# Performance work log

Hardware: AMD Instinct MI355X
Metric: run time of the kernel (lower is better)

The kernel has to match this reference:

```python
import jax, jax.numpy as jnp
import numpy as np

D_MODEL = 512
NHEAD = 8
HEAD_DIM = D_MODEL // NHEAD
D_FF = 2048
EPS = 1e-5


def _layernorm(x, w, b):
    mu = jnp.mean(x, axis=-1, keepdims=True)
    var = jnp.mean(jnp.square(x - mu), axis=-1, keepdims=True)
    return (x - mu) * jax.lax.rsqrt(var + EPS) * w + b


def setup_inputs() -> dict:
    key = jax.random.key(0)
    ks = jax.random.split(key, 10)
    B, L = 4, 2048
    x = jax.random.normal(ks[0], (B, L, D_MODEL), dtype=jnp.float32)
    attn_bias = jax.random.normal(ks[1], (1, NHEAD, L, L), dtype=jnp.float32)
    s = 0.02
    # weights stored as (in, out): y = x @ w + b
    wq = jax.random.normal(ks[2], (D_MODEL, D_MODEL), dtype=jnp.float32) * s
    wk = jax.random.normal(ks[3], (D_MODEL, D_MODEL), dtype=jnp.float32) * s
    wv = jax.random.normal(ks[4], (D_MODEL, D_MODEL), dtype=jnp.float32) * s
    wo = jax.random.normal(ks[5], (D_MODEL, D_MODEL), dtype=jnp.float32) * s
    w1 = jax.random.normal(ks[6], (D_MODEL, D_FF), dtype=jnp.float32) * s
    w2 = jax.random.normal(ks[7], (D_FF, D_MODEL), dtype=jnp.float32) * s
    z = lambda n: jnp.zeros((n,), dtype=jnp.float32)
    o = lambda n: jnp.ones((n,), dtype=jnp.float32)
    return {
        "x": x, "attn_bias": attn_bias,
        "ln1_w": o(D_MODEL), "ln1_b": z(D_MODEL),
        "ln2_w": o(D_MODEL), "ln2_b": z(D_MODEL),
        "wq": wq, "bq": z(D_MODEL), "wk": wk, "bk": z(D_MODEL),
        "wv": wv, "bv": z(D_MODEL), "wo": wo, "bo": z(D_MODEL),
        "w1": w1, "b1": z(D_FF), "w2": w2, "b2": z(D_MODEL),
    }


def reference(x, attn_bias, ln1_w, ln1_b, ln2_w, ln2_b,
              wq, bq, wk, bk, wv, bv, wo, bo, w1, b1, w2, b2):
    B, L, D = x.shape
    H, Dh = NHEAD, HEAD_DIM

    # --- self-attention block (pre-LN) ---
    h = _layernorm(x, ln1_w, ln1_b)
    q = (h @ wq + bq).reshape(B, L, H, Dh)
    k = (h @ wk + bk).reshape(B, L, H, Dh)
    v = (h @ wv + bv).reshape(B, L, H, Dh)
    scores = jnp.einsum('bqhd,bkhd->bhqk', q, k) * (Dh ** -0.5)
    scores = scores + attn_bias  # broadcast over batch if bias has leading 1
    attn = jax.nn.softmax(scores, axis=-1)
    o = jnp.einsum('bhqk,bkhd->bqhd', attn, v).reshape(B, L, D)
    x = x + (o @ wo + bo)

    # --- feed-forward block (pre-LN, exact GELU like torch nn.GELU) ---
    h2 = _layernorm(x, ln2_w, ln2_b)
    ff = jax.nn.gelu(h2 @ w1 + b1, approximate=False) @ w2 + b2
    return x + ff
```

## Files before the change

### kernel.cpp

```cpp
#include <hip/hip_runtime.h>
#include <hip/hip_bf16.h>

typedef __bf16 bf16x8 __attribute__((ext_vector_type(8)));
typedef float  f32x4  __attribute__((ext_vector_type(4)));
typedef unsigned short us8 __attribute__((ext_vector_type(8)));

__device__ inline unsigned short f2bf(float f) {
    unsigned u = __builtin_bit_cast(unsigned, f);
    u += 0x7fffu + ((u >> 16) & 1u);
    return (unsigned short)(u >> 16);
}

__device__ inline bf16x8 load_frag(const unsigned short* p) {
    return *reinterpret_cast<const bf16x8*>(p);
}

__device__ inline void gload_lds16(const unsigned short* g, unsigned short* l) {
    __builtin_amdgcn_global_load_lds(
        (const __attribute__((address_space(1))) void*)g,
        (__attribute__((address_space(3))) void*)l, 16, 0, 0);
}

__global__ void prep_kernel(const float* __restrict__ wq, const float* __restrict__ wk,
                            const float* __restrict__ wv, const float* __restrict__ wo,
                            const float* __restrict__ w1, const float* __restrict__ w2,
                            const float* __restrict__ bq, const float* __restrict__ bk,
                            const float* __restrict__ bv,
                            unsigned short* __restrict__ wqkvT, unsigned short* __restrict__ woT,
                            unsigned short* __restrict__ w1T, unsigned short* __restrict__ w2T,
                            float* __restrict__ biasqkv) {
    int bid = blockIdx.x;
    int tx = threadIdx.x, ty = threadIdx.y;
    if (bid >= 3072) {
        int i = (bid - 3072) * 256 + ty * 32 + tx;
        float v = (i < 512) ? bq[i] : ((i < 1024) ? bk[i - 512] : bv[i - 1024]);
        biasqkv[i] = v;
        return;
    }
    const float* src; unsigned short* dst; int K, N, tile;
    if (bid < 256)       { src = wq; dst = wqkvT;          K = 512;  N = 512;  tile = bid; }
    else if (bid < 512)  { src = wk; dst = wqkvT + 262144; K = 512;  N = 512;  tile = bid - 256; }
    else if (bid < 768)  { src = wv; dst = wqkvT + 524288; K = 512;  N = 512;  tile = bid - 512; }
    else if (bid < 1024) { src = wo; dst = woT;            K = 512;  N = 512;  tile = bid - 768; }
    else if (bid < 2048) { src = w1; dst = w1T;            K = 512;  N = 2048; tile = bid - 1024; }
    else                 { src = w2; dst = w2T;            K = 2048; N = 512;  tile = bid - 2048; }
    int ntx = N >> 5;
    int n0 = (tile % ntx) * 32, k0 = (tile / ntx) * 32;
    __shared__ float tilebuf[32][33];
#pragma unroll
    for (int i = 0; i < 4; ++i)
        tilebuf[ty + 8 * i][tx] = src[(size_t)(k0 + ty + 8 * i) * N + n0 + tx];
    __syncthreads();
#pragma unroll
    for (int i = 0; i < 4; ++i)
        dst[(size_t)(n0 + ty + 8 * i) * K + k0 + tx] = f2bf(tilebuf[tx][ty + 8 * i]);
}

__global__ __launch_bounds__(256) void ln_kernel(const float* __restrict__ x,
                                                 const float* __restrict__ w,
                                                 const float* __restrict__ b,
                                                 unsigned short* __restrict__ out) {
    int wave = threadIdx.x >> 6, lane = threadIdx.x & 63;
    size_t row = (size_t)blockIdx.x * 4 + wave;
    const float* xp = x + row * 512 + lane * 8;
    float4 v0 = *reinterpret_cast<const float4*>(xp);
    float4 v1 = *reinterpret_cast<const float4*>(xp + 4);
    float s = (v0.x + v0.y) + (v0.z + v0.w) + (v1.x + v1.y) + (v1.z + v1.w);
    float qq = v0.x * v0.x + v0.y * v0.y + v0.z * v0.z + v0.w * v0.w
             + v1.x * v1.x + v1.y * v1.y + v1.z * v1.z + v1.w * v1.w;
#pragma unroll
    for (int off = 1; off < 64; off <<= 1) {
        s += __shfl_xor(s, off, 64);
        qq += __shfl_xor(qq, off, 64);
    }
    float mu = s * (1.0f / 512.0f);
    float var = qq * (1.0f / 512.0f) - mu * mu;
    float rstd = rsqrtf(var + 1e-5f);
    int c = lane * 8;
    float4 w0 = *reinterpret_cast<const float4*>(w + c);
    float4 w1 = *reinterpret_cast<const float4*>(w + c + 4);
    float4 b0 = *reinterpret_cast<const float4*>(b + c);
    float4 b1 = *reinterpret_cast<const float4*>(b + c + 4);
    us8 r;
    r[0] = f2bf((v0.x - mu) * rstd * w0.x + b0.x);
    r[1] = f2bf((v0.y - mu) * rstd * w0.y + b0.y);
    r[2] = f2bf((v0.z - mu) * rstd * w0.z + b0.z);
    r[3] = f2bf((v0.w - mu) * rstd * w0.w + b0.w);
    r[4] = f2bf((v1.x - mu) * rstd * w1.x + b1.x);
    r[5] = f2bf((v1.y - mu) * rstd * w1.y + b1.y);
    r[6] = f2bf((v1.z - mu) * rstd * w1.z + b1.z);
    r[7] = f2bf((v1.w - mu) * rstd * w1.w + b1.w);
    *reinterpret_cast<us8*>(out + row * 512 + c) = r;
}

__device__ __forceinline__ void gemm_core(const unsigned short* __restrict__ A,
                                          const unsigned short* __restrict__ BT,
                                          int K, int kbeg, int ksteps,
                                          int m0, int n0, f32x4 (&acc)[4][4]) {
    __shared__ unsigned short As[8192];
    __shared__ unsigned short Bs[8192];
    const int tid = threadIdx.x;
    const int lane = tid & 63, wave = tid >> 6;
    const int quad = lane >> 4, l16 = lane & 15;
    const int wm = (wave >> 1) * 64, wn = (wave & 1) * 64;
    const int row0 = tid >> 3;
    const int jl = (tid & 7) ^ (row0 & 7);
    const unsigned short* ag = A + (size_t)(m0 + row0) * K + kbeg + jl * 8;
    const unsigned short* bg = BT + (size_t)(n0 + row0) * K + kbeg + jl * 8;
    unsigned short* al = As + tid * 8;
    unsigned short* bl = Bs + tid * 8;
    const int sw = l16 & 7;

    for (int ks = 0; ks < ksteps; ++ks) {
        __syncthreads();
#pragma unroll
        for (int s = 0; s < 4; ++s) {
            gload_lds16(ag + (size_t)32 * s * K, al + 2048 * s);
            gload_lds16(bg + (size_t)32 * s * K, bl + 2048 * s);
        }
        ag += 64; bg += 64;
        __syncthreads();
#pragma unroll
        for (int h = 0; h < 2; ++h) {
            bf16x8 af[4], bf[4];
#pragma unroll
            for (int i = 0; i < 4; ++i)
                af[i] = load_frag(As + (wm + i * 16 + l16) * 64 + (((h * 4 + quad) ^ sw) * 8));
#pragma unroll
            for (int j = 0; j < 4; ++j)
                bf[j] = load_frag(Bs + (wn + j * 16 + l16) * 64 + (((h * 4 + quad) ^ sw) * 8));
#pragma unroll
            for (int i = 0; i < 4; ++i)
#pragma unroll
                for (int j = 0; j < 4; ++j)
                    acc[i][j] = __builtin_amdgcn_mfma_f32_16x16x32_bf16(af[i], bf[j], acc[i][j], 0, 0, 0);
        }
    }
}

__global__ __launch_bounds__(256, 3) void gemm_qkv_k(const unsigned short* __restrict__ A,
                                                     const unsigned short* __restrict__ BT,
                                                     const float* __restrict__ bias,
                                                     unsigned short* __restrict__ qk,
                                                     unsigned short* __restrict__ vT) {
    f32x4 acc[4][4] = {};
    const int m0 = blockIdx.y * 128, n0 = blockIdx.x * 128;
    gemm_core(A, BT, 512, 0, 8, m0, n0, acc);
    const int tid = threadIdx.x, lane = tid & 63, wave = tid >> 6;
    const int quad = lane >> 4, l16 = lane & 15;
    const int wm = (wave >> 1) * 64, wn = (wave & 1) * 64;
    if (n0 < 1024) {
#pragma unroll
        for (int i = 0; i < 4; ++i)
#pragma unroll
            for (int j = 0; j < 4; ++j) {
                int n = n0 + wn + j * 16 + l16;
                float bn = bias[n];
#pragma unroll
                for (int r = 0; r < 4; ++r) {
                    int m = m0 + wm + i * 16 + quad * 4 + r;
                    qk[(size_t)m * 1024 + n] = f2bf(acc[i][j][r] + bn);
                }
            }
    } else {
#pragma unroll
        for (int i = 0; i < 4; ++i) {
            int mb = m0 + wm + i * 16 + quad * 4;
            int bb = mb >> 11, tok = mb & 2047;
#pragma unroll
            for (int j = 0; j < 4; ++j) {
                int n = n0 + wn + j * 16 + l16;
                float bn = bias[n];
                int hd = n - 1024;
                ushort4 pk;
                pk.x = f2bf(acc[i][j][0] + bn);
                pk.y = f2bf(acc[i][j][1] + bn);
                pk.z = f2bf(acc[i][j][2] + bn);
                pk.w = f2bf(acc[i][j][3] + bn);
                *reinterpret_cast<ushort4*>(vT + (size_t)(bb * 512 + hd) * 2048 + tok) = pk;
            }
        }
    }
}

__global__ __launch_bounds__(256, 3) void gemm_gelu_k(const unsigned short* __restrict__ A,
                                                      const unsigned short* __restrict__ BT,
                                                      const float* __restrict__ bias,
                                                      unsigned short* __restrict__ C) {
    f32x4 acc[4][4] = {};
    const int m0 = blockIdx.y * 128, n0 = blockIdx.x * 128;
    gemm_core(A, BT, 512, 0, 8, m0, n0, acc);
    const int tid = threadIdx.x, lane = tid & 63, wave = tid >> 6;
    const int quad = lane >> 4, l16 = lane & 15;
    const int wm = (wave >> 1) * 64, wn = (wave & 1) * 64;
#pragma unroll
    for (int i = 0; i < 4; ++i)
#pragma unroll
        for (int j = 0; j < 4; ++j) {
            int n = n0 + wn + j * 16 + l16;
            float bn = bias[n];
#pragma unroll
            for (int r = 0; r < 4; ++r) {
                int m = m0 + wm + i * 16 + quad * 4 + r;
                float val = acc[i][j][r] + bn;
                float g = 0.5f * val * (1.0f + erff(val * 0.70710678118654752f));
                C[(size_t)m * 2048 + n] = f2bf(g);
            }
        }
}

__global__ __launch_bounds__(256, 3) void gemm_atomic_k(const unsigned short* __restrict__ A,
                                                        const unsigned short* __restrict__ BT,
                                                        const float* __restrict__ bias,
                                                        float* __restrict__ C,
                                                        int N, int K, int ksteps) {
    f32x4 acc[4][4] = {};
    const int m0 = blockIdx.y * 128, n0 = blockIdx.x * 128;
    const int kbeg = blockIdx.z * ksteps * 64;
    gemm_core(A, BT, K, kbeg, ksteps, m0, n0, acc);
    const int tid = threadIdx.x, lane = tid & 63, wave = tid >> 6;
    const int quad = lane >> 4, l16 = lane & 15;
    const int wm = (wave >> 1) * 64, wn = (wave & 1) * 64;
    const bool addb = (blockIdx.z == 0);
#pragma unroll
    for (int i = 0; i < 4; ++i)
#pragma unroll
        for (int j = 0; j < 4; ++j) {
            int n = n0 + wn + j * 16 + l16;
            float bn = addb ? bias[n] : 0.0f;
#pragma unroll
            for (int r = 0; r < 4; ++r) {
                int m = m0 + wm + i * 16 + quad * 4 + r;
                atomicAdd(&C[(size_t)m * N + n], acc[i][j][r] + bn);
            }
        }
}

__global__ __launch_bounds__(256, 4) void attn_kernel(const unsigned short* __restrict__ qk,
                                                      const unsigned short* __restrict__ vT,
                                                      const float* __restrict__ bias,
                                                      unsigned short* __restrict__ o) {
    __shared__ unsigned short Ks[2][4096];
    __shared__ unsigned short VTs[2][4096];
    __shared__ unsigned short Ps[4096];
    const int tid = threadIdx.x;
    const int lane = tid & 63, wave = tid >> 6, quad = lane >> 4, l16 = lane & 15;
    const int qb = blockIdx.x, h = blockIdx.y, b = blockIdx.z;
    const int qw = qb * 64 + wave * 16;

    const unsigned short* qbase = qk + (size_t)(b * 2048 + qw + l16) * 1024 + h * 64 + quad * 8;
    bf16x8 qf0 = load_frag(qbase);
    bf16x8 qf1 = load_frag(qbase + 32);

    f32x4 Oacc[4] = {};
    float lsum[4] = {};

    const int p8 = lane & 7;
    const int r0 = wave * 16 + (lane >> 3);
    const int swz = (p8 ^ (r0 & 7)) * 8;
    const unsigned short* kg = qk + (size_t)(b * 2048 + r0) * 1024 + 512 + h * 64 + swz;
    const unsigned short* vg = vT + (size_t)(b * 512 + h * 64 + r0) * 2048 + swz;
    const int ldst = r0 * 64 + p8 * 8;

    const float* brow = bias + (size_t)h * 2048 * 2048 + (size_t)(qw + quad * 4) * 2048 + l16;
    const float S2 = 0.18033688011112042f;
    const float K2 = 1.4426950408889634f;
    const float C2 = -11.541560327111707f;

    gload_lds16(kg, Ks[0] + ldst);
    gload_lds16(kg + 8 * 1024, Ks[0] + 512 + ldst);
    gload_lds16(vg, VTs[0] + ldst);
    gload_lds16(vg + 8 * 2048, VTs[0] + 512 + ldst);
    float bbf[4][4];
#pragma unroll
    for (int t = 0; t < 4; ++t)
#pragma unroll
        for (int r = 0; r < 4; ++r)
            bbf[t][r] = fmaf(brow[(size_t)r * 2048 + t * 16], K2, C2);

    const int sw7 = l16 & 7;
    for (int kt = 0; kt < 32; ++kt) {
        const int buf = kt & 1;
        __syncthreads();
        if (kt < 31) {
            const unsigned short* kg2 = kg + (size_t)(kt + 1) * 64 * 1024;
            const unsigned short* vg2 = vg + (kt + 1) * 64;
            gload_lds16(kg2, Ks[buf ^ 1] + ldst);
            gload_lds16(kg2 + 8 * 1024, Ks[buf ^ 1] + 512 + ldst);
            gload_lds16(vg2, VTs[buf ^ 1] + ldst);
            gload_lds16(vg2 + 8 * 2048, VTs[buf ^ 1] + 512 + ldst);
        }
#pragma unroll
        for (int t = 0; t < 4; ++t) {
            const unsigned short* krow = Ks[buf] + (t * 16 + l16) * 64;
            bf16x8 kb0 = load_frag(krow + ((quad ^ sw7) * 8));
            bf16x8 kb1 = load_frag(krow + (((quad + 4) ^ sw7) * 8));
            f32x4 c = {};
            c = __builtin_amdgcn_mfma_f32_16x16x32_bf16(qf0, kb0, c, 0, 0, 0);
            c = __builtin_amdgcn_mfma_f32_16x16x32_bf16(qf1, kb1, c, 0, 0, 0);
#pragma unroll
            for (int r = 0; r < 4; ++r) {
                float e = __builtin_amdgcn_exp2f(fmaf(c[r], S2, bbf[t][r]));
                lsum[r] += e;
                int m = quad * 4 + r;
                int phys = (t * 2 + (l16 >> 3)) ^ ((m >> 1) & 7);
                Ps[wave * 1024 + m * 64 + phys * 8 + (l16 & 7)] = f2bf(e);
            }
        }
        __syncthreads();
        if (kt < 31) {
            const float* b2 = brow + (size_t)(kt + 1) * 64;
#pragma unroll
            for (int t = 0; t < 4; ++t)
#pragma unroll
                for (int r = 0; r < 4; ++r)
                    bbf[t][r] = fmaf(b2[(size_t)r * 2048 + t * 16], K2, C2);
        }
        const unsigned short* prow = Ps + wave * 1024 + l16 * 64;
        bf16x8 pa0 = load_frag(prow + ((quad ^ ((l16 >> 1) & 7)) * 8));
        bf16x8 pa1 = load_frag(prow + (((quad + 4) ^ ((l16 >> 1) & 7)) * 8));
#pragma unroll
        for (int t = 0; t < 4; ++t) {
            const unsigned short* vrow = VTs[buf] + (t * 16 + l16) * 64;
            bf16x8 vb0 = load_frag(vrow + ((quad ^ sw7) * 8));
            bf16x8 vb1 = load_frag(vrow + (((quad + 4) ^ sw7) * 8));
            Oacc[t] = __builtin_amdgcn_mfma_f32_16x16x32_bf16(pa0, vb0, Oacc[t], 0, 0, 0);
            Oacc[t] = __builtin_amdgcn_mfma_f32_16x16x32_bf16(pa1, vb1, Oacc[t], 0, 0, 0);
        }
    }

#pragma unroll
    for (int off = 1; off < 16; off <<= 1)
#pragma unroll
        for (int r = 0; r < 4; ++r) lsum[r] += __shfl_xor(lsum[r], off, 64);
#pragma unroll
    for (int r = 0; r < 4; ++r) {
        float inv = 1.0f / lsum[r];
        int qg = qw + quad * 4 + r;
        unsigned short* op = o + (size_t)(b * 2048 + qg) * 512 + h * 64;
#pragma unroll
        for (int t = 0; t < 4; ++t) op[t * 16 + l16] = f2bf(Oacc[t][r] * inv);
    }
}

extern "C" void kernel_launch(void* const* d_in, const int* in_sizes, int n_in,
                              void* d_out, int out_size, void* d_ws, size_t ws_size,
                              hipStream_t stream) {
    const float* x      = (const float*)d_in[0];
    const float* abias  = (const float*)d_in[1];
    const float* ln1_w  = (const float*)d_in[2];
    const float* ln1_b  = (const float*)d_in[3];
    const float* ln2_w  = (const float*)d_in[4];
    const float* ln2_b  = (const float*)d_in[5];
    const float* wq     = (const float*)d_in[6];
    const float* bq     = (const float*)d_in[7];
    const float* wk     = (const float*)d_in[8];
    const float* bk     = (const float*)d_in[9];
    const float* wv     = (const float*)d_in[10];
    const float* bv     = (const float*)d_in[11];
    const float* wo     = (const float*)d_in[12];
    const float* bo     = (const float*)d_in[13];
    const float* w1     = (const float*)d_in[14];
    const float* b1     = (const float*)d_in[15];
    const float* w2     = (const float*)d_in[16];
    const float* b2     = (const float*)d_in[17];
    float* out = (float*)d_out;

    char* ws = (char*)d_ws;
    unsigned short* wqkvT  = (unsigned short*)(ws + 0);
    unsigned short* woT    = (unsigned short*)(ws + 1572864);
    unsigned short* w1T    = (unsigned short*)(ws + 2097152);
    unsigned short* w2T    = (unsigned short*)(ws + 4194304);
    float*          biasqkv= (float*)(ws + 6291456);
    unsigned short* hbuf   = (unsigned short*)(ws + 6297600);
    unsigned short* qkbuf  = (unsigned short*)(ws + 14686208);
    unsigned short* vTbuf  = (unsigned short*)(ws + 31463424);
    unsigned short* o_attn = (unsigned short*)(ws + 39852032);
    unsigned short* ff1    = (unsigned short*)(ws + 48240640);

    hipMemcpyAsync(out, x, (size_t)8192 * 512 * sizeof(float), hipMemcpyDeviceToDevice, stream);
    prep_kernel<<<3078, dim3(32, 8), 0, stream>>>(wq, wk, wv, wo, w1, w2, bq, bk, bv,
                                                  wqkvT, woT, w1T, w2T, biasqkv);
    ln_kernel<<<2048, 256, 0, stream>>>(x, ln1_w, ln1_b, hbuf);
    gemm_qkv_k<<<dim3(12, 64), 256, 0, stream>>>(hbuf, wqkvT, biasqkv, qkbuf, vTbuf);
    attn_kernel<<<dim3(32, 8, 4), 256, 0, stream>>>(qkbuf, vTbuf, abias, o_attn);
    gemm_atomic_k<<<dim3(4, 64, 2), 256, 0, stream>>>(o_attn, woT, bo, out, 512, 512, 4);
    ln_kernel<<<2048, 256, 0, stream>>>(out, ln2_w, ln2_b, hbuf);
    gemm_gelu_k<<<dim3(16, 64), 256, 0, stream>>>(hbuf, w1T, b1, ff1);
    gemm_atomic_k<<<dim3(4, 64, 2), 256, 0, stream>>>(ff1, w2T, b2, out, 512, 2048, 16);
}
```

Before: 426.7 us.

## Share attention bias across batch pairs and replace split-K atomics with fused epilogues

The attention kernel now processes two batches per block so each attn_bias tile is loaded once and reused, halving bias traffic at the cost of more LDS and registers and half as many blocks. The split-K atomic GEMMs are replaced by 128x64-tile GEMMs that write directly, with the residual add fused into the output-projection epilogue, which removes the initial memcpy of x and the atomic traffic. The FF2 GEMM loses its K-split parallelism, and the occupancy hints in the launch bounds are dropped.

```diff
diff --git a/kernel.cpp b/kernel.cpp
--- a/kernel.cpp
+++ b/kernel.cpp
@@ -95,7 +95,7 @@
 
 __device__ __forceinline__ void gemm_core(const unsigned short* __restrict__ A,
                                           const unsigned short* __restrict__ BT,
-                                          int K, int kbeg, int ksteps,
+                                          int K, int ksteps,
                                           int m0, int n0, f32x4 (&acc)[4][4]) {
     __shared__ unsigned short As[8192];
     __shared__ unsigned short Bs[8192];
@@ -105,8 +105,8 @@
     const int wm = (wave >> 1) * 64, wn = (wave & 1) * 64;
     const int row0 = tid >> 3;
     const int jl = (tid & 7) ^ (row0 & 7);
-    const unsigned short* ag = A + (size_t)(m0 + row0) * K + kbeg + jl * 8;
-    const unsigned short* bg = BT + (size_t)(n0 + row0) * K + kbeg + jl * 8;
+    const unsigned short* ag = A + (size_t)(m0 + row0) * K + jl * 8;
+    const unsigned short* bg = BT + (size_t)(n0 + row0) * K + jl * 8;
     unsigned short* al = As + tid * 8;
     unsigned short* bl = Bs + tid * 8;
     const int sw = l16 & 7;
@@ -138,14 +138,114 @@
     }
 }
 
-__global__ __launch_bounds__(256, 3) void gemm_qkv_k(const unsigned short* __restrict__ A,
-                                                     const unsigned short* __restrict__ BT,
-                                                     const float* __restrict__ bias,
-                                                     unsigned short* __restrict__ qk,
-                                                     unsigned short* __restrict__ vT) {
+__device__ __forceinline__ void gemm_core_n64(const unsigned short* __restrict__ A,
+                                              const unsigned short* __restrict__ BT,
+                                              int K, int ksteps,
+                                              int m0, int n0, f32x4 (&acc)[2][4]) {
+    __shared__ unsigned short As[8192];
+    __shared__ unsigned short Bs[4096];
+    const int tid = threadIdx.x;
+    const int lane = tid & 63, wave = tid >> 6;
+    const int quad = lane >> 4, l16 = lane & 15;
+    const int wm = wave * 32;
+    const int row0 = tid >> 3;
+    const int jl = (tid & 7) ^ (row0 & 7);
+    const unsigned short* ag = A + (size_t)(m0 + row0) * K + jl * 8;
+    const unsigned short* bg = BT + (size_t)(n0 + (row0 & 31)) * K + jl * 8;
+    unsigned short* al = As + tid * 8;
+    unsigned short* bl = Bs + tid * 8;
+    const bool bstage = (row0 < 32);
+    (void)bstage;
+    const int sw = l16 & 7;
+
+    for (int ks = 0; ks < ksteps; ++ks) {
+        __syncthreads();
+#pragma unroll
+        for (int s = 0; s < 4; ++s)
+            gload_lds16(ag + (size_t)32 * s * K, al + 2048 * s);
+#pragma unroll
+        for (int s = 0; s < 2; ++s)
+            gload_lds16(bg + (size_t)32 * s * K, bl + 2048 * s);
+        ag += 64; bg += 64;
+        __syncthreads();
+#pragma unroll
+        for (int h = 0; h < 2; ++h) {
+            bf16x8 af[2], bf[4];
+#pragma unroll
+            for (int i = 0; i < 2; ++i)
+                af[i] = load_frag(As + (wm + i * 16 + l16) * 64 + (((h * 4 + quad) ^ sw) * 8));
+#pragma unroll
+            for (int j = 0; j < 4; ++j)
+                bf[j] = load_frag(Bs + (j * 16 + l16) * 64 + (((h * 4 + quad) ^ sw) * 8));
+#pragma unroll
+            for (int i = 0; i < 2; ++i)
+#pragma unroll
+                for (int j = 0; j < 4; ++j)
+                    acc[i][j] = __builtin_amdgcn_mfma_f32_16x16x32_bf16(af[i], bf[j], acc[i][j], 0, 0, 0);
+        }
+    }
+}
+
+
+__global__ __launch_bounds__(256) void gemm_oproj(const unsigned short* __restrict__ A,
+                                                  const unsigned short* __restrict__ BT,
+                                                  const float* __restrict__ bias,
+                                                  const float* __restrict__ res,
+                                                  float* __restrict__ C) {
+    f32x4 acc[2][4] = {};
+    const int m0 = blockIdx.y * 128, n0 = blockIdx.x * 64;
+    gemm_core_n64(A, BT, 512, 8, m0, n0, acc);
+    const int tid = threadIdx.x, lane = tid & 63, wave = tid >> 6;
+    const int quad = lane >> 4, l16 = lane & 15;
+    const int wm = wave * 32;
+#pragma unroll
+    for (int i = 0; i < 2; ++i)
+#pragma unroll
+        for (int j = 0; j < 4; ++j) {
+            int n = n0 + j * 16 + l16;
+            float bn = bias[n];
+#pragma unroll
+            for (int r = 0; r < 4; ++r) {
+                int m = m0 + wm + i * 16 + quad * 4 + r;
+                size_t idx = (size_t)m * 512 + n;
+                C[idx] = acc[i][j][r] + bn + res[idx];
+            }
+        }
+}
+
+__global__ __launch_bounds__(256) void gemm_ff2(const unsigned short* __restrict__ A,
+                                                const unsigned short* __restrict__ BT,
+                                                const float* __restrict__ bias,
+                                                float* __restrict__ C) {
+    f32x4 acc[2][4] = {};
+    const int m0 = blockIdx.y * 128, n0 = blockIdx.x * 64;
+    gemm_core_n64(A, BT, 2048, 32, m0, n0, acc);
+    const int tid = threadIdx.x, lane = tid & 63, wave = tid >> 6;
+    const int quad = lane >> 4, l16 = lane & 15;
+    const int wm = wave * 32;
+#pragma unroll
+    for (int i = 0; i < 2; ++i)
+#pragma unroll
+        for (int j = 0; j < 4; ++j) {
+            int n = n0 + j * 16 + l16;
+            float bn = bias[n];
+#pragma unroll
+            for (int r = 0; r < 4; ++r) {
+                int m = m0 + wm + i * 16 + quad * 4 + r;
+                size_t idx = (size_t)m * 512 + n;
+                C[idx] = C[idx] + acc[i][j][r] + bn;
+            }
+        }
+}
+
+__global__ __launch_bounds__(256) void gemm_qkv_k(const unsigned short* __restrict__ A,
+                                                  const unsigned short* __restrict__ BT,
+                                                  const float* __restrict__ bias,
+                                                  unsigned short* __restrict__ qk,
+                                                  unsigned short* __restrict__ vT) {
     f32x4 acc[4][4] = {};
     const int m0 = blockIdx.y * 128, n0 = blockIdx.x * 128;
-    gemm_core(A, BT, 512, 0, 8, m0, n0, acc);
+    gemm_core(A, BT, 512, 8, m0, n0, acc);
     const int tid = threadIdx.x, lane = tid & 63, wave = tid >> 6;
     const int quad = lane >> 4, l16 = lane & 15;
     const int wm = (wave >> 1) * 64, wn = (wave & 1) * 64;
@@ -183,13 +283,13 @@
     }
 }
 
-__global__ __launch_bounds__(256, 3) void gemm_gelu_k(const unsigned short* __restrict__ A,
-                                                      const unsigned short* __restrict__ BT,
-                                                      const float* __restrict__ bias,
-                                                      unsigned short* __restrict__ C) {
+__global__ __launch_bounds__(256) void gemm_gelu_k(const unsigned short* __restrict__ A,
+                                                   const unsigned short* __restrict__ BT,
+                                                   const float* __restrict__ bias,
+                                                   unsigned short* __restrict__ C) {
     f32x4 acc[4][4] = {};
     const int m0 = blockIdx.y * 128, n0 = blockIdx.x * 128;
-    gemm_core(A, BT, 512, 0, 8, m0, n0, acc);
+    gemm_core(A, BT, 512, 8, m0, n0, acc);
     const int tid = threadIdx.x, lane = tid & 63, wave = tid >> 6;
     const int quad = lane >> 4, l16 = lane & 15;
     const int wm = (wave >> 1) * 64, wn = (wave & 1) * 64;
@@ -209,57 +309,41 @@
         }
 }
 
-__global__ __launch_bounds__(256, 3) void gemm_atomic_k(const unsigned short* __restrict__ A,
-                                                        const unsigned short* __restrict__ BT,
-                                                        const float* __restrict__ bias,
-                                                        float* __restrict__ C,
-                                                        int N, int K, int ksteps) {
-    f32x4 acc[4][4] = {};
-    const int m0 = blockIdx.y * 128, n0 = blockIdx.x * 128;
-    const int kbeg = blockIdx.z * ksteps * 64;
-    gemm_core(A, BT, K, kbeg, ksteps, m0, n0, acc);
-    const int tid = threadIdx.x, lane = tid & 63, wave = tid >> 6;
-    const int quad = lane >> 4, l16 = lane & 15;
-    const int wm = (wave >> 1) * 64, wn = (wave & 1) * 64;
-    const bool addb = (blockIdx.z == 0);
-#pragma unroll
-    for (int i = 0; i < 4; ++i)
-#pragma unroll
-        for (int j = 0; j < 4; ++j) {
-            int n = n0 + wn + j * 16 + l16;
-            float bn = addb ? bias[n] : 0.0f;
-#pragma unroll
-            for (int r = 0; r < 4; ++r) {
-                int m = m0 + wm + i * 16 + quad * 4 + r;
-                atomicAdd(&C[(size_t)m * N + n], acc[i][j][r] + bn);
-            }
-        }
-}
-
-__global__ __launch_bounds__(256, 4) void attn_kernel(const unsigned short* __restrict__ qk,
-                                                      const unsigned short* __restrict__ vT,
-                                                      const float* __restrict__ bias,
-                                                      unsigned short* __restrict__ o) {
-    __shared__ unsigned short Ks[2][4096];
-    __shared__ unsigned short VTs[2][4096];
-    __shared__ unsigned short Ps[4096];
+__global__ __launch_bounds__(256) void attn_kernel(const unsigned short* __restrict__ qk,
+                                                   const unsigned short* __restrict__ vT,
+                                                   const float* __restrict__ bias,
+                                                   unsigned short* __restrict__ o) {
+    __shared__ unsigned short Ks[2][2][4096];
+    __shared__ unsigned short VTs[2][2][4096];
+    __shared__ unsigned short Ps[2][4096];
     const int tid = threadIdx.x;
     const int lane = tid & 63, wave = tid >> 6, quad = lane >> 4, l16 = lane & 15;
-    const int qb = blockIdx.x, h = blockIdx.y, b = blockIdx.z;
+    const int qb = blockIdx.x, h = blockIdx.y, bp = blockIdx.z;
     const int qw = qb * 64 + wave * 16;
 
-    const unsigned short* qbase = qk + (size_t)(b * 2048 + qw + l16) * 1024 + h * 64 + quad * 8;
-    bf16x8 qf0 = load_frag(qbase);
-    bf16x8 qf1 = load_frag(qbase + 32);
-
-    f32x4 Oacc[4] = {};
-    float lsum[4] = {};
+    bf16x8 qf[2][2];
+#pragma unroll
+    for (int bi = 0; bi < 2; ++bi) {
+        const unsigned short* qbase =
+            qk + (size_t)((bp * 2 + bi) * 2048 + qw + l16) * 1024 + h * 64 + quad * 8;
+        qf[bi][0] = load_frag(qbase);
+        qf[bi][1] = load_frag(qbase + 32);
+    }
+
+    f32x4 Oacc[2][4] = {};
+    float lsum[2][4] = {};
 
     const int p8 = lane & 7;
     const int r0 = wave * 16 + (lane >> 3);
     const int swz = (p8 ^ (r0 & 7)) * 8;
-    const unsigned short* kg = qk + (size_t)(b * 2048 + r0) * 1024 + 512 + h * 64 + swz;
-    const unsigned short* vg = vT + (size_t)(b * 512 + h * 64 + r0) * 2048 + swz;
+    const unsigned short* kg[2];
+    const unsigned short* vg[2];
+#pragma unroll
+    for (int bi = 0; bi < 2; ++bi) {
+        int b = bp * 2 + bi;
+        kg[bi] = qk + (size_t)(b * 2048 + r0) * 1024 + 512 + h * 64 + swz;
+        vg[bi] = vT + (size_t)(b * 512 + h * 64 + r0) * 2048 + swz;
+    }
     const int ldst = r0 * 64 + p8 * 8;
 
     const float* brow = bias + (size_t)h * 2048 * 2048 + (size_t)(qw + quad * 4) * 2048 + l16;
@@ -267,10 +351,13 @@
     const float K2 = 1.4426950408889634f;
     const float C2 = -11.541560327111707f;
 
-    gload_lds16(kg, Ks[0] + ldst);
-    gload_lds16(kg + 8 * 1024, Ks[0] + 512 + ldst);
-    gload_lds16(vg, VTs[0] + ldst);
-    gload_lds16(vg + 8 * 2048, VTs[0] + 512 + ldst);
+#pragma unroll
+    for (int bi = 0; bi < 2; ++bi) {
+        gload_lds16(kg[bi], &Ks[0][bi][0] + ldst);
+        gload_lds16(kg[bi] + 8 * 1024, &Ks[0][bi][512] + ldst);
+        gload_lds16(vg[bi], &VTs[0][bi][0] + ldst);
+        gload_lds16(vg[bi] + 8 * 2048, &VTs[0][bi][512] + ldst);
+    }
     float bbf[4][4];
 #pragma unroll
     for (int t = 0; t < 4; ++t)
@@ -283,28 +370,34 @@
         const int buf = kt & 1;
         __syncthreads();
         if (kt < 31) {
-            const unsigned short* kg2 = kg + (size_t)(kt + 1) * 64 * 1024;
-            const unsigned short* vg2 = vg + (kt + 1) * 64;
-            gload_lds16(kg2, Ks[buf ^ 1] + ldst);
-            gload_lds16(kg2 + 8 * 1024, Ks[buf ^ 1] + 512 + ldst);
-            gload_lds16(vg2, VTs[buf ^ 1] + ldst);
-            gload_lds16(vg2 + 8 * 2048, VTs[buf ^ 1] + 512 + ldst);
-        }
-#pragma unroll
-        for (int t = 0; t < 4; ++t) {
-            const unsigned short* krow = Ks[buf] + (t * 16 + l16) * 64;
-            bf16x8 kb0 = load_frag(krow + ((quad ^ sw7) * 8));
-            bf16x8 kb1 = load_frag(krow + (((quad + 4) ^ sw7) * 8));
-            f32x4 c = {};
-            c = __builtin_amdgcn_mfma_f32_16x16x32_bf16(qf0, kb0, c, 0, 0, 0);
-            c = __builtin_amdgcn_mfma_f32_16x16x32_bf16(qf1, kb1, c, 0, 0, 0);
-#pragma unroll
-            for (int r = 0; r < 4; ++r) {
-                float e = __builtin_amdgcn_exp2f(fmaf(c[r], S2, bbf[t][r]));
-                lsum[r] += e;
-                int m = quad * 4 + r;
-                int phys = (t * 2 + (l16 >> 3)) ^ ((m >> 1) & 7);
-                Ps[wave * 1024 + m * 64 + phys * 8 + (l16 & 7)] = f2bf(e);
+#pragma unroll
+            for (int bi = 0; bi < 2; ++bi) {
+                const unsigned short* kg2 = kg[bi] + (size_t)(kt + 1) * 64 * 1024;
+                const unsigned short* vg2 = vg[bi] + (kt + 1) * 64;
+                gload_lds16(kg2, &Ks[buf ^ 1][bi][0] + ldst);
+                gload_lds16(kg2 + 8 * 1024, &Ks[buf ^ 1][bi][512] + ldst);
+                gload_lds16(vg2, &VTs[buf ^ 1][bi][0] + ldst);
+                gload_lds16(vg2 + 8 * 2048, &VTs[buf ^ 1][bi][512] + ldst);
+            }
+        }
+#pragma unroll
+        for (int bi = 0; bi < 2; ++bi) {
+#pragma unroll
+            for (int t = 0; t < 4; ++t) {
+                const unsigned short* krow = &Ks[buf][bi][(t * 16 + l16) * 64];
+                bf16x8 kb0 = load_frag(krow + ((quad ^ sw7) * 8));
+                bf16x8 kb1 = load_frag(krow + (((quad + 4) ^ sw7) * 8));
+                f32x4 c = {};
+                c = __builtin_amdgcn_mfma_f32_16x16x32_bf16(qf[bi][0], kb0, c, 0, 0, 0);
+                c = __builtin_amdgcn_mfma_f32_16x16x32_bf16(qf[bi][1], kb1, c, 0, 0, 0);
+#pragma unroll
+                for (int r = 0; r < 4; ++r) {
+                    float e = __builtin_amdgcn_exp2f(fmaf(c[r], S2, bbf[t][r]));
+                    lsum[bi][r] += e;
+                    int m = quad * 4 + r;
+                    int phys = (t * 2 + (l16 >> 3)) ^ ((m >> 1) & 7);
+                    Ps[bi][wave * 1024 + m * 64 + phys * 8 + (l16 & 7)] = f2bf(e);
+                }
             }
         }
         __syncthreads();
@@ -316,31 +409,38 @@
                 for (int r = 0; r < 4; ++r)
                     bbf[t][r] = fmaf(b2[(size_t)r * 2048 + t * 16], K2, C2);
         }
-        const unsigned short* prow = Ps + wave * 1024 + l16 * 64;
-        bf16x8 pa0 = load_frag(prow + ((quad ^ ((l16 >> 1) & 7)) * 8));
-        bf16x8 pa1 = load_frag(prow + (((quad + 4) ^ ((l16 >> 1) & 7)) * 8));
-#pragma unroll
-        for (int t = 0; t < 4; ++t) {
-            const unsigned short* vrow = VTs[buf] + (t * 16 + l16) * 64;
-            bf16x8 vb0 = load_frag(vrow + ((quad ^ sw7) * 8));
-            bf16x8 vb1 = load_frag(vrow + (((quad + 4) ^ sw7) * 8));
-            Oacc[t] = __builtin_amdgcn_mfma_f32_16x16x32_bf16(pa0, vb0, Oacc[t], 0, 0, 0);
-            Oacc[t] = __builtin_amdgcn_mfma_f32_16x16x32_bf16(pa1, vb1, Oacc[t], 0, 0, 0);
+#pragma unroll
+        for (int bi = 0; bi < 2; ++bi) {
+            const unsigned short* prow = &Ps[bi][wave * 1024 + l16 * 64];
+            bf16x8 pa0 = load_frag(prow + ((quad ^ ((l16 >> 1) & 7)) * 8));
+            bf16x8 pa1 = load_frag(prow + (((quad + 4) ^ ((l16 >> 1) & 7)) * 8));
+#pragma unroll
+            for (int t = 0; t < 4; ++t) {
+                const unsigned short* vrow = &VTs[buf][bi][(t * 16 + l16) * 64];
+                bf16x8 vb0 = load_frag(vrow + ((quad ^ sw7) * 8));
+                bf16x8 vb1 = load_frag(vrow + (((quad + 4) ^ sw7) * 8));
+                Oacc[bi][t] = __builtin_amdgcn_mfma_f32_16x16x32_bf16(pa0, vb0, Oacc[bi][t], 0, 0, 0);
+                Oacc[bi][t] = __builtin_amdgcn_mfma_f32_16x16x32_bf16(pa1, vb1, Oacc[bi][t], 0, 0, 0);
+            }
         }
     }
 
 #pragma unroll
     for (int off = 1; off < 16; off <<= 1)
 #pragma unroll
-        for (int r = 0; r < 4; ++r) lsum[r] += __shfl_xor(lsum[r], off, 64);
-#pragma unroll
-    for (int r = 0; r < 4; ++r) {
-        float inv = 1.0f / lsum[r];
-        int qg = qw + quad * 4 + r;
-        unsigned short* op = o + (size_t)(b * 2048 + qg) * 512 + h * 64;
-#pragma unroll
-        for (int t = 0; t < 4; ++t) op[t * 16 + l16] = f2bf(Oacc[t][r] * inv);
-    }
+        for (int bi = 0; bi < 2; ++bi)
+#pragma unroll
+            for (int r = 0; r < 4; ++r) lsum[bi][r] += __shfl_xor(lsum[bi][r], off, 64);
+#pragma unroll
+    for (int bi = 0; bi < 2; ++bi)
+#pragma unroll
+        for (int r = 0; r < 4; ++r) {
+            float inv = 1.0f / lsum[bi][r];
+            int qg = qw + quad * 4 + r;
+            unsigned short* op = o + (size_t)((bp * 2 + bi) * 2048 + qg) * 512 + h * 64;
+#pragma unroll
+            for (int t = 0; t < 4; ++t) op[t * 16 + l16] = f2bf(Oacc[bi][t][r] * inv);
+        }
 }
 
 extern "C" void kernel_launch(void* const* d_in, const int* in_sizes, int n_in,
@@ -378,14 +478,13 @@
     unsigned short* o_attn = (unsigned short*)(ws + 39852032);
     unsigned short* ff1    = (unsigned short*)(ws + 48240640);
 
-    hipMemcpyAsync(out, x, (size_t)8192 * 512 * sizeof(float), hipMemcpyDeviceToDevice, stream);
     prep_kernel<<<3078, dim3(32, 8), 0, stream>>>(wq, wk, wv, wo, w1, w2, bq, bk, bv,
                                                   wqkvT, woT, w1T, w2T, biasqkv);
     ln_kernel<<<2048, 256, 0, stream>>>(x, ln1_w, ln1_b, hbuf);
     gemm_qkv_k<<<dim3(12, 64), 256, 0, stream>>>(hbuf, wqkvT, biasqkv, qkbuf, vTbuf);
-    attn_kernel<<<dim3(32, 8, 4), 256, 0, stream>>>(qkbuf, vTbuf, abias, o_attn);
-    gemm_atomic_k<<<dim3(4, 64, 2), 256, 0, stream>>>(o_attn, woT, bo, out, 512, 512, 4);
+    attn_kernel<<<dim3(32, 8, 2), 256, 0, stream>>>(qkbuf, vTbuf, abias, o_attn);
+    gemm_oproj<<<dim3(8, 64), 256, 0, stream>>>(o_attn, woT, bo, x, out);
     ln_kernel<<<2048, 256, 0, stream>>>(out, ln2_w, ln2_b, hbuf);
     gemm_gelu_k<<<dim3(16, 64), 256, 0, stream>>>(hbuf, w1T, b1, ff1);
-    gemm_atomic_k<<<dim3(4, 64, 2), 256, 0, stream>>>(ff1, w2T, b2, out, 512, 2048, 16);
-}
+    gemm_ff2<<<dim3(8, 64), 256, 0, stream>>>(ff1, w2T, b2, out);
+}
```

Result: faster. 417.0 us (-2.3%).
